# Optimization experiments

Measured on AMD Instinct MI355X. Metric: run time of the kernel, lower is better.

Reference implementation:

```python
import jax, jax.numpy as jnp
import numpy as np

EMBED = 1024
DFF = 4096


def _layernorm(x, g, b, eps=1e-5):
    mu = jnp.mean(x, axis=-1, keepdims=True)
    var = jnp.var(x, axis=-1, keepdims=True)
    return (x - mu) * jax.lax.rsqrt(var + eps) * g + b


def setup_inputs() -> dict:
    key = jax.random.key(0)
    ks = jax.random.split(key, 14)
    s = 1.0 / np.sqrt(EMBED)
    sf = 1.0 / np.sqrt(DFF)
    d = {
        "src": jax.random.normal(ks[0], (4, 2048, EMBED), dtype=jnp.float32),
        "Wq": jax.random.uniform(ks[1], (EMBED, EMBED), jnp.float32, -s, s),
        "bq": jnp.zeros((EMBED,), jnp.float32),
        "Wk": jax.random.uniform(ks[2], (EMBED, EMBED), jnp.float32, -s, s),
        "bk": jnp.zeros((EMBED,), jnp.float32),
        "Wv": jax.random.uniform(ks[3], (EMBED, EMBED), jnp.float32, -s, s),
        "bv": jnp.zeros((EMBED,), jnp.float32),
        "Wo": jax.random.uniform(ks[4], (EMBED, EMBED), jnp.float32, -s, s),
        "bo": jnp.zeros((EMBED,), jnp.float32),
        "W1": jax.random.uniform(ks[5], (EMBED, DFF), jnp.float32, -s, s),
        "b1": jnp.zeros((DFF,), jnp.float32),
        "W2": jax.random.uniform(ks[6], (DFF, EMBED), jnp.float32, -sf, sf),
        "b2": jnp.zeros((EMBED,), jnp.float32),
        "g1": jnp.ones((EMBED,), jnp.float32),
        "be1": jnp.zeros((EMBED,), jnp.float32),
        "g2": jnp.ones((EMBED,), jnp.float32),
        "be2": jnp.zeros((EMBED,), jnp.float32),
    }
    return d


def reference(src, Wq, bq, Wk, bk, Wv, bv, Wo, bo, W1, b1, W2, b2, g1, be1, g2, be2):
    # Q/K/V projections: [b, s, d]
    Q = src @ Wq + bq
    K = src @ Wk + bk
    V = src @ Wv + bv
    # Single-head, UNSCALED attention (faithful to source: no 1/sqrt(d), num_heads unused)
    scores = jnp.einsum("bqd,bkd->bqk", Q, K)  # [b, s, s]
    weights = jax.nn.softmax(scores, axis=-1)
    attn = jnp.einsum("bqk,bkd->bqd", weights, V)
    attn = attn @ Wo + bo
    x = _layernorm(src + attn, g1, be1)
    ff = jax.nn.relu(x @ W1 + b1) @ W2 + b2
    return _layernorm(x + ff, g2, be2)
```

## Files before the change

### kernel.cpp

```cpp
#include <hip/hip_runtime.h>
#include <stdint.h>

typedef unsigned short u16;
typedef _Float16 v8h __attribute__((ext_vector_type(8)));
typedef float v4f __attribute__((ext_vector_type(4)));

static __device__ __forceinline__ float h2f(u16 u) {
    union { u16 s; _Float16 h; } v; v.s = u; return (float)v.h;
}
static __device__ __forceinline__ u16 f2h(float f) {
    union { u16 s; _Float16 h; } v; v.h = (_Float16)f; return v.s;
}

static __device__ __forceinline__ void gload_lds16(const u16* g, const u16* l) {
    __builtin_amdgcn_global_load_lds(
        (const __attribute__((address_space(1))) uint32_t*)(uintptr_t)g,
        (__attribute__((address_space(3))) uint32_t*)(uintptr_t)l,
        16, 0, 0);
}

__global__ __launch_bounds__(256) void cvt_f16(const float* __restrict__ in,
                                               u16* __restrict__ out, int n8) {
    const int i = blockIdx.x * 256 + threadIdx.x;
    if (i >= n8) return;
    const float4 a = ((const float4*)in)[2 * i];
    const float4 b = ((const float4*)in)[2 * i + 1];
    u16 o[8] = {f2h(a.x), f2h(a.y), f2h(a.z), f2h(a.w),
                f2h(b.x), f2h(b.y), f2h(b.z), f2h(b.w)};
    *(uint4*)(out + (size_t)i * 8) = *(const uint4*)o;
}

__global__ __launch_bounds__(256) void transpose_all(
    const float* __restrict__ Wq, const float* __restrict__ Wk,
    const float* __restrict__ Wv, const float* __restrict__ Wo,
    const float* __restrict__ W1, const float* __restrict__ W2,
    u16* __restrict__ WqkvT, u16* __restrict__ WoT,
    u16* __restrict__ W1T, u16* __restrict__ W2T)
{
    int t = blockIdx.x;
    const float* in; u16* out; long ldi, ldo; int xt;
    if (t < 1024)      {            in = Wq; out = WqkvT;               ldi = 1024; ldo = 1024; xt = 32; }
    else if (t < 2048) { t -= 1024; in = Wk; out = WqkvT + 1024*1024;   ldi = 1024; ldo = 1024; xt = 32; }
    else if (t < 3072) { t -= 2048; in = Wv; out = WqkvT + 2*1024*1024; ldi = 1024; ldo = 1024; xt = 32; }
    else if (t < 4096) { t -= 3072; in = Wo; out = WoT;                 ldi = 1024; ldo = 1024; xt = 32; }
    else if (t < 8192) { t -= 4096; in = W1; out = W1T;                 ldi = 4096; ldo = 1024; xt = 128; }
    else               { t -= 8192; in = W2; out = W2T;                 ldi = 1024; ldo = 4096; xt = 32; }
    const int c0 = (t % xt) * 32, r0 = (t / xt) * 32;
    __shared__ float tile[32][33];
    for (int i = threadIdx.y; i < 32; i += 8)
        tile[i][threadIdx.x] = in[(long)(r0 + i) * ldi + c0 + threadIdx.x];
    __syncthreads();
    for (int i = threadIdx.y; i < 32; i += 8)
        out[(long)(c0 + i) * ldo + r0 + threadIdx.x] = f2h(tile[threadIdx.x][i]);
}

template<int OMODE, int BIAS, bool RELU, int NX, int NY, int NZ>
__global__ __launch_bounds__(256) void gemm_f16(
    const u16* __restrict__ A, long lda, long Asb,
    const u16* __restrict__ B, long ldb, long Bsb,
    void* __restrict__ Cv, long ldc, long Csb, u16* __restrict__ C1,
    const float* __restrict__ bias, const float* __restrict__ bias2,
    const float* __restrict__ bias3, int K)
{
    static_assert((NY * NZ) % 8 == 0, "Y-band remap needs NY*NZ % 8 == 0");
    alignas(16) __shared__ u16 As[128 * 64];
    alignas(16) __shared__ u16 Bs[128 * 64];
    const int t = threadIdx.x;

    const int lin = blockIdx.x + NX * (blockIdx.y + NY * blockIdx.z);
    const int g = lin & 7;
    const int s = lin >> 3;
    const int xe = s % NX;
    const int yl = s / NX;
    const int Y = g * (NY * NZ / 8) + yl;
    const int ye = Y % NY;
    const long b = Y / NY;

    A += b * Asb; B += b * Bsb;
    const long m0 = (long)ye * 128;
    const long n0 = (long)xe * 128;
    const int lane = t & 63, wave = t >> 6;
    const int wm = (wave >> 1) * 64, wn = (wave & 1) * 64;
    const int l16 = lane & 15, quad = lane >> 4;

    const int rr = t >> 3;
    const int cg8 = ((t & 7) ^ ((t >> 3) & 7)) * 8;
    const int wv512 = wave * 512;

    long aofs[4], bofs[4];
#pragma unroll
    for (int p = 0; p < 4; ++p) {
        aofs[p] = (m0 + p * 32 + rr) * lda + cg8;
        bofs[p] = (n0 + p * 32 + rr) * ldb + cg8;
    }

    v4f acc[4][4];
#pragma unroll
    for (int i = 0; i < 4; ++i)
#pragma unroll
        for (int j = 0; j < 4; ++j)
            acc[i][j] = (v4f){0.f, 0.f, 0.f, 0.f};

    for (int k0 = 0; k0 < K; k0 += 64) {
        __syncthreads();
#pragma unroll
        for (int p = 0; p < 4; ++p) {
            gload_lds16(A + aofs[p] + k0, As + p * 2048 + wv512);
            gload_lds16(B + bofs[p] + k0, Bs + p * 2048 + wv512);
        }
        __syncthreads();

#pragma unroll
        for (int kk = 0; kk < 2; ++kk) {
            const int swz = ((kk * 4 + quad) ^ (l16 & 7)) * 8;
            v8h af[4], bfr[4];
#pragma unroll
            for (int i = 0; i < 4; ++i)
                af[i] = *(const v8h*)&As[(wm + i * 16 + l16) * 64 + swz];
#pragma unroll
            for (int j = 0; j < 4; ++j)
                bfr[j] = *(const v8h*)&Bs[(wn + j * 16 + l16) * 64 + swz];
#pragma unroll
            for (int i = 0; i < 4; ++i)
#pragma unroll
                for (int j = 0; j < 4; ++j)
                    acc[i][j] = __builtin_amdgcn_mfma_f32_16x16x32_f16(af[i], bfr[j], acc[i][j], 0, 0, 0);
        }
    }

    float bv[4];
#pragma unroll
    for (int j = 0; j < 4; ++j) {
        const long col = n0 + wn + j * 16 + l16;
        if (BIAS == 0) bv[j] = 0.f;
        else if (BIAS == 1) bv[j] = bias[col];
        else {
            const int sel = (int)(col >> 10);
            const float* bp = sel == 0 ? bias : (sel == 1 ? bias2 : bias3);
            bv[j] = bp[col & 1023];
        }
    }

    if (OMODE == 3 && n0 >= 2048) {
        const long bb = m0 >> 11, mb = m0 & 2047;
        u16* C = C1 + bb * Csb;
#pragma unroll
        for (int j = 0; j < 4; ++j) {
            const long col = n0 - 2048 + wn + j * 16 + l16;
            u16* pc = C + col * 2048 + mb + wm + quad * 4;
#pragma unroll
            for (int i = 0; i < 4; ++i) {
                u16 o[4];
#pragma unroll
                for (int r = 0; r < 4; ++r) {
                    float val = acc[i][j][r] + bv[j];
                    if (RELU) val = fmaxf(val, 0.f);
                    o[r] = f2h(val);
                }
                *(uint2*)(pc + i * 16) = *(const uint2*)o;
            }
        }
    } else {
        const long cb = b * ((OMODE == 3) ? 0 : Csb) + (m0 + wm + quad * 4) * ldc + (n0 + wn + l16);
        u16* p0 = (u16*)Cv + cb;
#pragma unroll
        for (int i = 0; i < 4; ++i)
#pragma unroll
            for (int r = 0; r < 4; ++r) {
                u16* prow = p0 + (long)(i * 16 + r) * ldc;
#pragma unroll
                for (int j = 0; j < 4; ++j) {
                    float val = acc[i][j][r] + bv[j];
                    if (RELU) val = fmaxf(val, 0.f);
                    prow[j * 16] = f2h(val);
                }
            }
    }
}

__global__ __launch_bounds__(256) void softmax_rows(u16* __restrict__ S) {
    const long row = blockIdx.x;
    u16* p = S + row * 2048;
    const int t = threadIdx.x;
    float v[8];
    float mx = -1e30f;
#pragma unroll
    for (int i = 0; i < 8; ++i) { v[i] = h2f(p[t + i * 256]); mx = fmaxf(mx, v[i]); }
    __shared__ float red[256];
    red[t] = mx; __syncthreads();
    for (int off = 128; off > 0; off >>= 1) {
        if (t < off) red[t] = fmaxf(red[t], red[t + off]);
        __syncthreads();
    }
    mx = red[0]; __syncthreads();
    float sum = 0.f;
#pragma unroll
    for (int i = 0; i < 8; ++i) { v[i] = __expf(v[i] - mx); sum += v[i]; }
    red[t] = sum; __syncthreads();
    for (int off = 128; off > 0; off >>= 1) {
        if (t < off) red[t] += red[t + off];
        __syncthreads();
    }
    const float inv = 1.f / red[0];
#pragma unroll
    for (int i = 0; i < 8; ++i) p[t + i * 256] = f2h(v[i] * inv);
}

__global__ __launch_bounds__(256) void ln_one(
    const float* __restrict__ a, const u16* __restrict__ bb,
    const float* __restrict__ g, const float* __restrict__ be,
    u16* __restrict__ out16)
{
    const long base = (long)blockIdx.x * 1024;
    const int t = threadIdx.x;
    float v[4]; float s = 0.f, ss = 0.f;
#pragma unroll
    for (int i = 0; i < 4; ++i) {
        const int c = t + i * 256;
        const float x = a[base + c] + h2f(bb[base + c]);
        v[i] = x; s += x; ss += x * x;
    }
    __shared__ float rs[256], rss[256];
    rs[t] = s; rss[t] = ss; __syncthreads();
    for (int off = 128; off > 0; off >>= 1) {
        if (t < off) { rs[t] += rs[t + off]; rss[t] += rss[t + off]; }
        __syncthreads();
    }
    const float mean = rs[0] * (1.f / 1024.f);
    const float var = rss[0] * (1.f / 1024.f) - mean * mean;
    const float rstd = rsqrtf(var + 1e-5f);
#pragma unroll
    for (int i = 0; i < 4; ++i) {
        const int c = t + i * 256;
        out16[base + c] = f2h((v[i] - mean) * rstd * g[c] + be[c]);
    }
}

__global__ __launch_bounds__(256) void ln_two(
    const u16* __restrict__ a, const u16* __restrict__ bb,
    const float* __restrict__ g, const float* __restrict__ be,
    float* __restrict__ out)
{
    const long base = (long)blockIdx.x * 1024;
    const int t = threadIdx.x;
    float v[4]; float s = 0.f, ss = 0.f;
#pragma unroll
    for (int i = 0; i < 4; ++i) {
        const int c = t + i * 256;
        const float x = h2f(a[base + c]) + h2f(bb[base + c]);
        v[i] = x; s += x; ss += x * x;
    }
    __shared__ float rs[256], rss[256];
    rs[t] = s; rss[t] = ss; __syncthreads();
    for (int off = 128; off > 0; off >>= 1) {
        if (t < off) { rs[t] += rs[t + off]; rss[t] += rss[t + off]; }
        __syncthreads();
    }
    const float mean = rs[0] * (1.f / 1024.f);
    const float var = rss[0] * (1.f / 1024.f) - mean * mean;
    const float rstd = rsqrtf(var + 1e-5f);
#pragma unroll
    for (int i = 0; i < 4; ++i) {
        const int c = t + i * 256;
        out[base + c] = (v[i] - mean) * rstd * g[c] + be[c];
    }
}

extern "C" void kernel_launch(void* const* d_in, const int* in_sizes, int n_in,
                              void* d_out, int out_size, void* d_ws, size_t ws_size,
                              hipStream_t stream) {
    (void)in_sizes; (void)n_in; (void)out_size; (void)ws_size;
    constexpr long S = 2048, E = 1024, F = 4096, M = 8192;

    const float* src = (const float*)d_in[0];
    const float* Wq  = (const float*)d_in[1];
    const float* bq  = (const float*)d_in[2];
    const float* Wk  = (const float*)d_in[3];
    const float* bk  = (const float*)d_in[4];
    const float* Wv  = (const float*)d_in[5];
    const float* bv  = (const float*)d_in[6];
    const float* Wo  = (const float*)d_in[7];
    const float* bo  = (const float*)d_in[8];
    const float* W1  = (const float*)d_in[9];
    const float* b1  = (const float*)d_in[10];
    const float* W2  = (const float*)d_in[11];
    const float* b2  = (const float*)d_in[12];
    const float* g1  = (const float*)d_in[13];
    const float* be1 = (const float*)d_in[14];
    const float* g2  = (const float*)d_in[15];
    const float* be2 = (const float*)d_in[16];

    char* ws = (char*)d_ws;
    size_t off = 0;
    auto take = [&](size_t bytes) {
        char* p = ws + off;
        off += (bytes + 255) & ~(size_t)255;
        return p;
    };
    const size_t MB16 = 16777216;
    u16*   srcH  = (u16*)take(MB16);
    u16*   WqkvT = (u16*)take(3 * E * E * 2);
    u16*   WoT   = (u16*)take(E * E * 2);
    u16*   W1T   = (u16*)take(F * E * 2);
    u16*   W2T   = (u16*)take(E * F * 2);
    char*  B0    = take(2 * MB16);
    char*  B1    = take(MB16);
    char*  B2    = take(4ull * S * S * 4);
    char*  B3    = take(MB16);
    char*  B4    = take(MB16);

    u16*   QK    = (u16*)B0;
    u16*   VT    = (u16*)B1;
    u16*   Sh    = (u16*)B2;
    u16*   hf    = (u16*)B2;
    u16*   attn  = (u16*)B3;
    u16*   xh    = (u16*)B3;
    u16*   attnO = (u16*)B4;
    u16*   ffO   = (u16*)B4;

    dim3 blk(256), tb(32, 8);

    cvt_f16<<<dim3(M * E / 8 / 256), blk, 0, stream>>>(src, srcH, M * E / 8);

    transpose_all<<<dim3(12288), tb, 0, stream>>>(Wq, Wk, Wv, Wo, W1, W2,
                                                  WqkvT, WoT, W1T, W2T);

    gemm_f16<3, 3, false, 24, 64, 1><<<dim3(24, 64, 1), blk, 0, stream>>>(
        srcH, E, 0, WqkvT, E, 0, QK, 2 * E, E * S, VT, bq, bk, bv, E);

    gemm_f16<0, 0, false, 16, 16, 4><<<dim3(16, 16, 4), blk, 0, stream>>>(
        QK, 2 * E, S * 2 * E, QK + E, 2 * E, S * 2 * E,
        Sh, S, S * S, nullptr, nullptr, nullptr, nullptr, E);

    softmax_rows<<<dim3(M), blk, 0, stream>>>(Sh);

    gemm_f16<0, 0, false, 8, 16, 4><<<dim3(8, 16, 4), blk, 0, stream>>>(
        Sh, S, S * S, VT, S, E * S,
        attn, E, S * E, nullptr, nullptr, nullptr, nullptr, S);

    gemm_f16<0, 1, false, 8, 64, 1><<<dim3(8, 64, 1), blk, 0, stream>>>(
        attn, E, 0, WoT, E, 0, attnO, E, 0, nullptr, bo, nullptr, nullptr, E);

    ln_one<<<dim3(M), blk, 0, stream>>>(src, attnO, g1, be1, xh);

    gemm_f16<0, 1, true, 32, 64, 1><<<dim3(32, 64, 1), blk, 0, stream>>>(
        xh, E, 0, W1T, E, 0, hf, F, 0, nullptr, b1, nullptr, nullptr, E);

    gemm_f16<0, 1, false, 8, 64, 1><<<dim3(8, 64, 1), blk, 0, stream>>>(
        hf, F, 0, W2T, F, 0, ffO, E, 0, nullptr, b2, nullptr, nullptr, F);

    ln_two<<<dim3(M), blk, 0, stream>>>(xh, ffO, g2, be2, (float*)d_out);
}
```

Before: 558.5 us.

## Add 256x256-tile 512-thread GEMM with XCD swizzle for QKV, scores, FFN1

Introduces a new GEMM kernel using 256x256 output tiles with 8 waves, a 4-slot LDS ring fed by direct global-to-LDS loads, swizzled LDS layout, and phase-interleaved MFMA with priority bumps. The workgroup index is remapped so consecutive tiles land on the same XCD for L2 reuse. It is applied to the QKV projection, QK^T scores and FFN1 GEMMs to raise arithmetic intensity and overlap loads with compute. Larger tiles reduce the number of workgroups, which may leave CUs idle or cause tail imbalance, and register pressure from 128 accumulators per thread may limit occupancy.

```diff
diff --git a/kernel.cpp b/kernel.cpp
--- a/kernel.cpp
+++ b/kernel.cpp
@@ -178,6 +178,177 @@
     }
 }
 
+template<int OMODE, int BIAS, bool RELU, int NX, int NY, int NZ>
+__global__ __launch_bounds__(512) void gemm256(
+    const u16* __restrict__ A, long lda, long Asb,
+    const u16* __restrict__ B, long ldb, long Bsb,
+    void* __restrict__ Cv, long ldc, long Csb, u16* __restrict__ C1,
+    const float* __restrict__ bias, const float* __restrict__ bias2,
+    const float* __restrict__ bias3, int K)
+{
+    constexpr int NWG = NX * NY * NZ;
+    static_assert(NWG % 8 == 0, "XCD swizzle needs nwg % 8 == 0");
+    alignas(16) __shared__ u16 As[4 * 8192];
+    alignas(16) __shared__ u16 Bs[4 * 8192];
+
+    const int tid = threadIdx.x;
+    const int lane = tid & 63, wave = tid >> 6;
+    const int l16 = lane & 15, quad = lane >> 4;
+    const int wm = wave >> 2;
+    const int wn = wave & 3;
+
+    const int lin = blockIdx.x;
+    const int tl = (lin & 7) * (NWG / 8) + (lin >> 3);
+    const int xe = tl % NX;
+    const int ye = (tl / NX) % NY;
+    const int zb = tl / (NX * NY);
+    const long m0 = (long)ye * 256;
+    const long n0 = (long)xe * 256;
+
+    const u16* Aop = A + (long)zb * Asb;
+    const u16* Bop = B + (long)zb * Bsb;
+
+    const int srow = tid >> 2;
+    const int sq = (tid & 3) ^ ((tid >> 3) & 3);
+    const long gaofs0 = (m0 + srow) * lda + sq * 8;
+    const long gaofs1 = gaofs0 + 128 * lda;
+    const long gbofs0 = (n0 + srow) * ldb + sq * 8;
+    const long gbofs1 = gbofs0 + 128 * ldb;
+    const int wv512n = wave * 512;
+
+    const int swzE = (quad ^ ((l16 >> 1) & 3)) * 8;
+    const int aRow = (wm * 128 + l16) * 32 + swzE;
+    const int bRow = (wn * 64 + l16) * 32 + swzE;
+
+    v4f acc[8][4];
+#pragma unroll
+    for (int i = 0; i < 8; ++i)
+#pragma unroll
+        for (int j = 0; j < 4; ++j)
+            acc[i][j] = (v4f){0.f, 0.f, 0.f, 0.f};
+    v8h bf[4];
+
+#define STAGE_A(RIDX, KP) do { \
+        u16* lb_ = As + (RIDX) * 8192 + wv512n; \
+        gload_lds16(Aop + gaofs0 + (KP), lb_); \
+        gload_lds16(Aop + gaofs1 + (KP), lb_ + 4096); } while (0)
+#define STAGE_B(RIDX, KP) do { \
+        u16* lb_ = Bs + (RIDX) * 8192 + wv512n; \
+        gload_lds16(Bop + gbofs0 + (KP), lb_); \
+        gload_lds16(Bop + gbofs1 + (KP), lb_ + 4096); } while (0)
+
+#define MF(CH, I, J) \
+    acc[(CH) * 4 + (I)][J] = __builtin_amdgcn_mfma_f32_16x16x32_f16( \
+        af##I, bf[J], acc[(CH) * 4 + (I)][J], 0, 0, 0)
+
+#define PHASE(BUF, KH, CH, EVENW, ...) { \
+        if (EVENW) asm volatile("s_waitcnt vmcnt(6)" ::: "memory"); \
+        const u16* Ar_ = As + ((BUF) * 2 + (KH)) * 8192 + aRow + (CH) * 2048; \
+        v8h af0 = *(const v8h*)(Ar_); \
+        v8h af1 = *(const v8h*)(Ar_ + 512); \
+        v8h af2 = *(const v8h*)(Ar_ + 1024); \
+        v8h af3 = *(const v8h*)(Ar_ + 1536); \
+        if ((CH) == 0) { \
+            const u16* Br_ = Bs + ((BUF) * 2 + (KH)) * 8192 + bRow; \
+            bf[0] = *(const v8h*)(Br_); \
+            bf[1] = *(const v8h*)(Br_ + 512); \
+            bf[2] = *(const v8h*)(Br_ + 1024); \
+            bf[3] = *(const v8h*)(Br_ + 1536); \
+        } \
+        __VA_ARGS__; \
+        __builtin_amdgcn_s_barrier(); \
+        asm volatile("s_waitcnt lgkmcnt(0)" ::: "memory"); \
+        __builtin_amdgcn_s_setprio(1); \
+        MF(CH,0,0); MF(CH,0,1); MF(CH,0,2); MF(CH,0,3); \
+        MF(CH,1,0); MF(CH,1,1); MF(CH,1,2); MF(CH,1,3); \
+        MF(CH,2,0); MF(CH,2,1); MF(CH,2,2); MF(CH,2,3); \
+        MF(CH,3,0); MF(CH,3,1); MF(CH,3,2); MF(CH,3,3); \
+        __builtin_amdgcn_s_setprio(0); \
+        __builtin_amdgcn_s_barrier(); \
+    }
+
+    STAGE_A(0, 0);  STAGE_B(0, 0);
+    STAGE_A(1, 32); STAGE_B(1, 32);
+    STAGE_A(2, 64); STAGE_B(2, 64);
+    asm volatile("s_waitcnt vmcnt(8)" ::: "memory");
+    __builtin_amdgcn_s_barrier();
+
+    const int NT = K >> 7;
+#pragma unroll 1
+    for (int t = 0; t < NT; ++t) {
+        const bool nl = (t < NT - 1);
+        const long kb = (long)t * 128;
+        const long kp1 = kb + 96;
+        const long kp2 = kb + 128;
+        const long kp2b = kb + 160;
+        const long kp3 = kb + 192;
+
+        PHASE(0, 0, 0, false, STAGE_A(3, kp1))
+        PHASE(0, 0, 1, true,  STAGE_B(3, kp1))
+        PHASE(0, 1, 0, false, if (nl) STAGE_A(0, kp2))
+        PHASE(0, 1, 1, true,  if (nl) STAGE_B(0, kp2))
+        PHASE(1, 0, 0, false, if (nl) STAGE_A(1, kp2b))
+        PHASE(1, 0, 1, true,  if (nl) STAGE_B(1, kp2b))
+        PHASE(1, 1, 0, false, if (nl) STAGE_A(2, kp3))
+        PHASE(1, 1, 1, true,  if (nl) STAGE_B(2, kp3))
+    }
+
+#undef PHASE
+#undef MF
+#undef STAGE_A
+#undef STAGE_B
+
+    float bv[4];
+#pragma unroll
+    for (int j = 0; j < 4; ++j) {
+        const long col = n0 + wn * 64 + j * 16 + l16;
+        if (BIAS == 0) bv[j] = 0.f;
+        else if (BIAS == 1) bv[j] = bias[col];
+        else {
+            const int sel = (int)(col >> 10);
+            const float* bp = sel == 0 ? bias : (sel == 1 ? bias2 : bias3);
+            bv[j] = bp[col & 1023];
+        }
+    }
+
+    if (OMODE == 3 && n0 >= 2048) {
+        const long bb = m0 >> 11, mb = m0 & 2047;
+        u16* C = C1 + bb * Csb;
+#pragma unroll
+        for (int j = 0; j < 4; ++j) {
+            const long col = n0 - 2048 + wn * 64 + j * 16 + l16;
+            u16* pc = C + col * 2048 + mb + wm * 128 + quad * 4;
+#pragma unroll
+            for (int i = 0; i < 8; ++i) {
+                u16 o[4];
+#pragma unroll
+                for (int r = 0; r < 4; ++r) {
+                    float val = acc[i][j][r] + bv[j];
+                    if (RELU) val = fmaxf(val, 0.f);
+                    o[r] = f2h(val);
+                }
+                *(uint2*)(pc + i * 16) = *(const uint2*)o;
+            }
+        }
+    } else {
+        const long cb = (OMODE == 3 ? 0 : (long)zb * Csb)
+                      + (m0 + wm * 128 + quad * 4) * ldc + (n0 + wn * 64 + l16);
+        u16* p0 = (u16*)Cv + cb;
+#pragma unroll
+        for (int i = 0; i < 8; ++i)
+#pragma unroll
+            for (int r = 0; r < 4; ++r) {
+                u16* prow = p0 + (long)(i * 16 + r) * ldc;
+#pragma unroll
+                for (int j = 0; j < 4; ++j) {
+                    float val = acc[i][j][r] + bv[j];
+                    if (RELU) val = fmaxf(val, 0.f);
+                    prow[j * 16] = f2h(val);
+                }
+            }
+    }
+}
+
 __global__ __launch_bounds__(256) void softmax_rows(u16* __restrict__ S) {
     const long row = blockIdx.x;
     u16* p = S + row * 2048;
@@ -318,17 +489,17 @@
     u16*   attnO = (u16*)B4;
     u16*   ffO   = (u16*)B4;
 
-    dim3 blk(256), tb(32, 8);
+    dim3 blk(256), blk5(512), tb(32, 8);
 
     cvt_f16<<<dim3(M * E / 8 / 256), blk, 0, stream>>>(src, srcH, M * E / 8);
 
     transpose_all<<<dim3(12288), tb, 0, stream>>>(Wq, Wk, Wv, Wo, W1, W2,
                                                   WqkvT, WoT, W1T, W2T);
 
-    gemm_f16<3, 3, false, 24, 64, 1><<<dim3(24, 64, 1), blk, 0, stream>>>(
+    gemm256<3, 3, false, 12, 32, 1><<<dim3(12 * 32), blk5, 0, stream>>>(
         srcH, E, 0, WqkvT, E, 0, QK, 2 * E, E * S, VT, bq, bk, bv, E);
 
-    gemm_f16<0, 0, false, 16, 16, 4><<<dim3(16, 16, 4), blk, 0, stream>>>(
+    gemm256<0, 0, false, 8, 8, 4><<<dim3(8 * 8 * 4), blk5, 0, stream>>>(
         QK, 2 * E, S * 2 * E, QK + E, 2 * E, S * 2 * E,
         Sh, S, S * S, nullptr, nullptr, nullptr, nullptr, E);
 
@@ -343,7 +514,7 @@
 
     ln_one<<<dim3(M), blk, 0, stream>>>(src, attnO, g1, be1, xh);
 
-    gemm_f16<0, 1, true, 32, 64, 1><<<dim3(32, 64, 1), blk, 0, stream>>>(
+    gemm256<0, 1, true, 16, 32, 1><<<dim3(16 * 32), blk5, 0, stream>>>(
         xh, E, 0, W1T, E, 0, hf, F, 0, nullptr, b1, nullptr, nullptr, E);
 
     gemm_f16<0, 1, false, 8, 64, 1><<<dim3(8, 64, 1), blk, 0, stream>>>(
```

New measurement: 527.2 us. 5.6% less time.

## Replace GEMM with 256x128-tile, 512-thread, multi-stage pipelined LDS kernel

Applied to the files above, without the earlier changes.

The 128x128 single-buffered GEMM, which waited on a barrier every K step, is replaced by a 512-thread kernel computing 256x128 tiles. A and B K-slices are staged into multiple LDS buffers ahead of use, and vmcnt waits, split barriers and s_setprio are used so global loads overlap the MFMA work. A 1D grid with XCD-aware swizzling maps tiles to chips. The larger tiles improve operand reuse and the deeper prefetch hides memory latency, at the cost of more LDS, fewer workgroups on the smaller GEMMs, and fragile hand-written wait counts.

```diff
diff --git a/kernel.cpp b/kernel.cpp
--- a/kernel.cpp
+++ b/kernel.cpp
@@ -55,44 +55,45 @@
 }
 
 template<int OMODE, int BIAS, bool RELU, int NX, int NY, int NZ>
-__global__ __launch_bounds__(256) void gemm_f16(
+__global__ __launch_bounds__(512, 4) void gemm256n(
     const u16* __restrict__ A, long lda, long Asb,
     const u16* __restrict__ B, long ldb, long Bsb,
     void* __restrict__ Cv, long ldc, long Csb, u16* __restrict__ C1,
     const float* __restrict__ bias, const float* __restrict__ bias2,
     const float* __restrict__ bias3, int K)
 {
-    static_assert((NY * NZ) % 8 == 0, "Y-band remap needs NY*NZ % 8 == 0");
-    alignas(16) __shared__ u16 As[128 * 64];
-    alignas(16) __shared__ u16 Bs[128 * 64];
-    const int t = threadIdx.x;
-
-    const int lin = blockIdx.x + NX * (blockIdx.y + NY * blockIdx.z);
-    const int g = lin & 7;
-    const int s = lin >> 3;
-    const int xe = s % NX;
-    const int yl = s / NX;
-    const int Y = g * (NY * NZ / 8) + yl;
-    const int ye = Y % NY;
-    const long b = Y / NY;
-
-    A += b * Asb; B += b * Bsb;
-    const long m0 = (long)ye * 128;
+    constexpr int NWG = NX * NY * NZ;
+    static_assert(NWG % 8 == 0, "XCD swizzle needs nwg % 8 == 0");
+    alignas(16) __shared__ u16 As[4 * 8192];
+    alignas(16) __shared__ u16 Bs[2 * 4096];
+
+    const int tid = threadIdx.x;
+    const int lane = tid & 63, wave = tid >> 6;
+    const int l16 = lane & 15, quad = lane >> 4;
+    const int wm = wave >> 1;
+    const int wn = wave & 1;
+
+    const int lin = blockIdx.x;
+    const int tl = (lin & 7) * (NWG / 8) + (lin >> 3);
+    const int xe = tl % NX;
+    const int ye = (tl / NX) % NY;
+    const int zb = tl / (NX * NY);
+    const long m0 = (long)ye * 256;
     const long n0 = (long)xe * 128;
-    const int lane = t & 63, wave = t >> 6;
-    const int wm = (wave >> 1) * 64, wn = (wave & 1) * 64;
-    const int l16 = lane & 15, quad = lane >> 4;
-
-    const int rr = t >> 3;
-    const int cg8 = ((t & 7) ^ ((t >> 3) & 7)) * 8;
-    const int wv512 = wave * 512;
-
-    long aofs[4], bofs[4];
-#pragma unroll
-    for (int p = 0; p < 4; ++p) {
-        aofs[p] = (m0 + p * 32 + rr) * lda + cg8;
-        bofs[p] = (n0 + p * 32 + rr) * ldb + cg8;
-    }
+
+    const u16* Aop = A + (long)zb * Asb;
+    const u16* Bop = B + (long)zb * Bsb;
+
+    const int srow = tid >> 2;
+    const int sq = (tid & 3) ^ ((tid >> 3) & 3);
+    const long gaofs0 = (m0 + srow) * lda + sq * 8;
+    const long gaofs1 = gaofs0 + 128 * lda;
+    const long gbofs0 = (n0 + srow) * ldb + sq * 8;
+    const int wv512n = wave * 512;
+
+    const int swzE = (quad ^ ((l16 >> 1) & 3)) * 8;
+    const int aRow = (wm * 64 + l16) * 32 + swzE;
+    const int bRow = (wn * 64 + l16) * 32 + swzE;
 
     v4f acc[4][4];
 #pragma unroll
@@ -100,38 +101,78 @@
 #pragma unroll
         for (int j = 0; j < 4; ++j)
             acc[i][j] = (v4f){0.f, 0.f, 0.f, 0.f};
-
-    for (int k0 = 0; k0 < K; k0 += 64) {
-        __syncthreads();
-#pragma unroll
-        for (int p = 0; p < 4; ++p) {
-            gload_lds16(A + aofs[p] + k0, As + p * 2048 + wv512);
-            gload_lds16(B + bofs[p] + k0, Bs + p * 2048 + wv512);
-        }
-        __syncthreads();
-
-#pragma unroll
-        for (int kk = 0; kk < 2; ++kk) {
-            const int swz = ((kk * 4 + quad) ^ (l16 & 7)) * 8;
-            v8h af[4], bfr[4];
-#pragma unroll
-            for (int i = 0; i < 4; ++i)
-                af[i] = *(const v8h*)&As[(wm + i * 16 + l16) * 64 + swz];
-#pragma unroll
-            for (int j = 0; j < 4; ++j)
-                bfr[j] = *(const v8h*)&Bs[(wn + j * 16 + l16) * 64 + swz];
-#pragma unroll
-            for (int i = 0; i < 4; ++i)
-#pragma unroll
-                for (int j = 0; j < 4; ++j)
-                    acc[i][j] = __builtin_amdgcn_mfma_f32_16x16x32_f16(af[i], bfr[j], acc[i][j], 0, 0, 0);
-        }
-    }
+    v8h bf[4];
+
+#define STAGE_A(RIDX, KP) do { \
+        u16* lb_ = As + (RIDX) * 8192 + wv512n; \
+        gload_lds16(Aop + gaofs0 + (KP), lb_); \
+        gload_lds16(Aop + gaofs1 + (KP), lb_ + 4096); } while (0)
+#define STAGE_B(SLOT, KP) do { \
+        gload_lds16(Bop + gbofs0 + (KP), Bs + (SLOT) * 4096 + wv512n); } while (0)
+
+#define PHASE(BUF, KH, CH, EVENW, STG) { \
+        if (EVENW) asm volatile("s_waitcnt vmcnt(2)" ::: "memory"); \
+        const u16* Ar_ = As + ((BUF) * 2 + (KH)) * 8192 + aRow + (CH) * 1024; \
+        v8h af0 = *(const v8h*)(Ar_); \
+        v8h af1 = *(const v8h*)(Ar_ + 512); \
+        if ((CH) == 0) { \
+            const u16* Br_ = Bs + (KH) * 4096 + bRow; \
+            bf[0] = *(const v8h*)(Br_); \
+            bf[1] = *(const v8h*)(Br_ + 512); \
+            bf[2] = *(const v8h*)(Br_ + 1024); \
+            bf[3] = *(const v8h*)(Br_ + 1536); \
+        } \
+        STG; \
+        __builtin_amdgcn_s_barrier(); \
+        asm volatile("s_waitcnt lgkmcnt(0)" ::: "memory"); \
+        __builtin_amdgcn_s_setprio(1); \
+        acc[(CH)*2+0][0] = __builtin_amdgcn_mfma_f32_16x16x32_f16(af0, bf[0], acc[(CH)*2+0][0], 0, 0, 0); \
+        acc[(CH)*2+0][1] = __builtin_amdgcn_mfma_f32_16x16x32_f16(af0, bf[1], acc[(CH)*2+0][1], 0, 0, 0); \
+        acc[(CH)*2+0][2] = __builtin_amdgcn_mfma_f32_16x16x32_f16(af0, bf[2], acc[(CH)*2+0][2], 0, 0, 0); \
+        acc[(CH)*2+0][3] = __builtin_amdgcn_mfma_f32_16x16x32_f16(af0, bf[3], acc[(CH)*2+0][3], 0, 0, 0); \
+        acc[(CH)*2+1][0] = __builtin_amdgcn_mfma_f32_16x16x32_f16(af1, bf[0], acc[(CH)*2+1][0], 0, 0, 0); \
+        acc[(CH)*2+1][1] = __builtin_amdgcn_mfma_f32_16x16x32_f16(af1, bf[1], acc[(CH)*2+1][1], 0, 0, 0); \
+        acc[(CH)*2+1][2] = __builtin_amdgcn_mfma_f32_16x16x32_f16(af1, bf[2], acc[(CH)*2+1][2], 0, 0, 0); \
+        acc[(CH)*2+1][3] = __builtin_amdgcn_mfma_f32_16x16x32_f16(af1, bf[3], acc[(CH)*2+1][3], 0, 0, 0); \
+        __builtin_amdgcn_s_setprio(0); \
+        __builtin_amdgcn_s_barrier(); \
+    }
+
+    STAGE_A(0, 0);  STAGE_B(0, 0);
+    STAGE_A(1, 32); STAGE_B(1, 32);
+    STAGE_A(2, 64);
+    asm volatile("s_waitcnt vmcnt(5)" ::: "memory");
+    __builtin_amdgcn_s_barrier();
+
+    const int NT = K >> 7;
+#pragma unroll 1
+    for (int t = 0; t < NT; ++t) {
+        const long kb = (long)t * 128;
+        long kp2  = kb + 128; if (kp2  >= K) kp2  = 0;
+        long kp2b = kb + 160; if (kp2b >= K) kp2b = 0;
+        long kp3  = kb + 192; if (kp3  >= K) kp3  = 0;
+
+        PHASE(0, 0, 0, false, STAGE_A(3, kb + 96))
+        PHASE(0, 0, 1, true,  STAGE_B(0, kb + 64))
+        PHASE(0, 1, 0, false, STAGE_A(0, kp2))
+        PHASE(0, 1, 1, true,  STAGE_B(1, kb + 96))
+        PHASE(1, 0, 0, false, STAGE_A(1, kp2b))
+        PHASE(1, 0, 1, true,  STAGE_B(0, kp2))
+        PHASE(1, 1, 0, false, STAGE_A(2, kp3))
+        PHASE(1, 1, 1, true,  STAGE_B(1, kp2b))
+    }
+
+    asm volatile("s_waitcnt vmcnt(0) lgkmcnt(0)" ::: "memory");
+    __builtin_amdgcn_s_barrier();
+
+#undef PHASE
+#undef STAGE_A
+#undef STAGE_B
 
     float bv[4];
 #pragma unroll
     for (int j = 0; j < 4; ++j) {
-        const long col = n0 + wn + j * 16 + l16;
+        const long col = n0 + wn * 64 + j * 16 + l16;
         if (BIAS == 0) bv[j] = 0.f;
         else if (BIAS == 1) bv[j] = bias[col];
         else {
@@ -146,8 +187,8 @@
         u16* C = C1 + bb * Csb;
 #pragma unroll
         for (int j = 0; j < 4; ++j) {
-            const long col = n0 - 2048 + wn + j * 16 + l16;
-            u16* pc = C + col * 2048 + mb + wm + quad * 4;
+            const long col = n0 - 2048 + wn * 64 + j * 16 + l16;
+            u16* pc = C + col * 2048 + mb + wm * 64 + quad * 4;
 #pragma unroll
             for (int i = 0; i < 4; ++i) {
                 u16 o[4];
@@ -161,7 +202,8 @@
             }
         }
     } else {
-        const long cb = b * ((OMODE == 3) ? 0 : Csb) + (m0 + wm + quad * 4) * ldc + (n0 + wn + l16);
+        const long cb = (OMODE == 3 ? 0 : (long)zb * Csb)
+                      + (m0 + wm * 64 + quad * 4) * ldc + (n0 + wn * 64 + l16);
         u16* p0 = (u16*)Cv + cb;
 #pragma unroll
         for (int i = 0; i < 4; ++i)
@@ -318,35 +360,35 @@
     u16*   attnO = (u16*)B4;
     u16*   ffO   = (u16*)B4;
 
-    dim3 blk(256), tb(32, 8);
+    dim3 blk(256), blk5(512), tb(32, 8);
 
     cvt_f16<<<dim3(M * E / 8 / 256), blk, 0, stream>>>(src, srcH, M * E / 8);
 
     transpose_all<<<dim3(12288), tb, 0, stream>>>(Wq, Wk, Wv, Wo, W1, W2,
                                                   WqkvT, WoT, W1T, W2T);
 
-    gemm_f16<3, 3, false, 24, 64, 1><<<dim3(24, 64, 1), blk, 0, stream>>>(
+    gemm256n<3, 3, false, 24, 32, 1><<<dim3(24 * 32), blk5, 0, stream>>>(
         srcH, E, 0, WqkvT, E, 0, QK, 2 * E, E * S, VT, bq, bk, bv, E);
 
-    gemm_f16<0, 0, false, 16, 16, 4><<<dim3(16, 16, 4), blk, 0, stream>>>(
+    gemm256n<0, 0, false, 16, 8, 4><<<dim3(16 * 8 * 4), blk5, 0, stream>>>(
         QK, 2 * E, S * 2 * E, QK + E, 2 * E, S * 2 * E,
         Sh, S, S * S, nullptr, nullptr, nullptr, nullptr, E);
 
     softmax_rows<<<dim3(M), blk, 0, stream>>>(Sh);
 
-    gemm_f16<0, 0, false, 8, 16, 4><<<dim3(8, 16, 4), blk, 0, stream>>>(
+    gemm256n<0, 0, false, 8, 8, 4><<<dim3(8 * 8 * 4), blk5, 0, stream>>>(
         Sh, S, S * S, VT, S, E * S,
         attn, E, S * E, nullptr, nullptr, nullptr, nullptr, S);
 
-    gemm_f16<0, 1, false, 8, 64, 1><<<dim3(8, 64, 1), blk, 0, stream>>>(
+    gemm256n<0, 1, false, 8, 32, 1><<<dim3(8 * 32), blk5, 0, stream>>>(
         attn, E, 0, WoT, E, 0, attnO, E, 0, nullptr, bo, nullptr, nullptr, E);
 
     ln_one<<<dim3(M), blk, 0, stream>>>(src, attnO, g1, be1, xh);
 
-    gemm_f16<0, 1, true, 32, 64, 1><<<dim3(32, 64, 1), blk, 0, stream>>>(
+    gemm256n<0, 1, true, 32, 32, 1><<<dim3(32 * 32), blk5, 0, stream>>>(
         xh, E, 0, W1T, E, 0, hf, F, 0, nullptr, b1, nullptr, nullptr, E);
 
-    gemm_f16<0, 1, false, 8, 64, 1><<<dim3(8, 64, 1), blk, 0, stream>>>(
+    gemm256n<0, 1, false, 8, 32, 1><<<dim3(8 * 32), blk5, 0, stream>>>(
         hf, F, 0, W2T, F, 0, ffO, E, 0, nullptr, b2, nullptr, nullptr, F);
 
     ln_two<<<dim3(M), blk, 0, stream>>>(xh, ffO, g2, be2, (float*)d_out);
```

Result: faster. 496.2 us (-11.2%).
